# Performance work log

Measured on AMD Instinct MI355X. Metric: run time of the kernel, lower is better.

Reference implementation:

```python
import jax, jax.numpy as jnp
import numpy as np

QMIN = 0.1
EPS = 1e-7
NN, NP_, NE = 200_000, 5_000, 10_000_000


def setup_inputs() -> dict:
    key = jax.random.key(0)
    ks = jax.random.split(key, 8)
    beta = jax.random.uniform(ks[0], (NN,), jnp.float32)
    x = jax.random.normal(ks[1], (NN, 3), jnp.float32)
    isTrack = jax.random.randint(ks[2], (NN,), 0, 2, jnp.int32)
    pt = jax.random.randint(ks[3], (NN,), 0, NP_, jnp.int32)
    noise = jax.random.uniform(ks[4], (NN,)) < 0.1
    parent_target = jnp.where(noise, -1, pt).astype(jnp.int32)
    particle_idx = jnp.arange(NP_, dtype=jnp.int32)
    particle_class = jax.random.randint(ks[5], (NP_,), 0, 5, jnp.int32)
    edge_node = jax.random.randint(ks[6], (NE,), 0, NN, jnp.int32)
    edge_particle = jax.random.randint(ks[7], (NE,), 0, NP_, jnp.int32)
    return {"beta": beta, "x": x, "isTrack": isTrack, "parent_target": parent_target,
            "particle_idx": particle_idx, "particle_class": particle_class,
            "edge_node": edge_node, "edge_particle": edge_particle}


def reference(beta, x, isTrack, parent_target, particle_idx, particle_class, edge_node, edge_particle):
    E = edge_node.shape[0]
    Nn = beta.shape[0]
    Np = particle_idx.shape[0]
    f32 = beta.dtype

    # edge label: node's parent target == particle's idx (ApplyTo*EdgeLabel)
    label = (parent_target[edge_node] == particle_idx[edge_particle]).astype(f32)

    # condensation charge q = arctanh(clamped beta)^2 + qmin
    cb = jnp.clip(beta, EPS, 1.0 - EPS)
    q = jnp.arctanh(cb) ** 2 + QMIN

    # ---- ChildToParent mailbox (masked gathers on edges) ----
    betas = beta[edge_node] * label                              # [E]
    track_m = isTrack[edge_node].astype(f32) * label             # [E]
    pclass_m = particle_class[edge_particle].astype(f32) * label  # [E]
    # where(parent_class < 2, betas, isTrack*betas)
    beta_mail = jnp.where(pclass_m < 2.0, betas, track_m * betas)

    # ---- per-particle max-beta reduction with argmax payload selection ----
    # init 'max beta'/'max q'/'max x' are zeros, concatenated first in the torch code
    max_beta = jax.ops.segment_max(beta_mail, edge_particle, num_segments=Np)
    max_beta = jnp.maximum(max_beta, 0.0)
    hit = (beta_mail == max_beta[edge_particle]) & (max_beta[edge_particle] > 0.0)
    winner = jnp.where(hit, jnp.arange(E, dtype=jnp.int32), -1)
    best_edge = jax.ops.segment_max(winner, edge_particle, num_segments=Np)
    valid = best_edge >= 0
    safe = jnp.maximum(best_edge, 0)
    qs = q[edge_node] * label
    xs = x[edge_node] * label[:, None]
    max_q = jnp.where(valid, qs[safe], 0.0)            # [Np]
    max_x = jnp.where(valid[:, None], xs[safe], 0.0)   # [Np,3]

    # ---- ParentToChild potentials (ParentToChildEF) ----
    diff = max_x[edge_particle] - x[edge_node]          # [E,3]
    dist = jnp.sqrt(jnp.sum(diff * diff, axis=1))       # [E]
    mq = max_q[edge_particle]
    v_attract = 3.0 * label * mq * dist * dist
    v_repulse = (1.0 - label) * jnp.maximum(2.0 - dist, 0.0) * mq

    # ---- sum mailbox to nodes (ParentToChildNF) ----
    attract = jax.ops.segment_sum(v_attract, edge_node, num_segments=Nn)
    repulse = jax.ops.segment_sum(v_repulse, edge_node, num_segments=Nn)
    node_lv = q * (attract + repulse)                   # [Nn]
    return node_lv
```

## Files before the change

### kernel.cpp

```cpp
#include <hip/hip_runtime.h>

#define QMIN_V 0.1f
#define EPS_V  1e-7f


__global__ void init_ws_kernel(unsigned long long* __restrict__ packed,
                               float* __restrict__ accum, int np, int nn) {
    int tid = blockIdx.x * blockDim.x + threadIdx.x;
    int stride = gridDim.x * blockDim.x;
    for (int j = tid; j < np; j += stride) packed[j] = 0ULL;
    for (int j = tid; j < nn; j += stride) accum[j] = 0.0f;
}

__global__ void passA_kernel(const int* __restrict__ edge_node,
                             const int* __restrict__ edge_particle,
                             const float* __restrict__ beta,
                             const int* __restrict__ isTrack,
                             const int* __restrict__ parent_target,
                             const int* __restrict__ particle_idx,
                             const int* __restrict__ particle_class,
                             unsigned long long* __restrict__ packed,
                             int ne4, int ne) {
    int tid = blockIdx.x * blockDim.x + threadIdx.x;
    int stride = gridDim.x * blockDim.x;
    for (int i = tid; i < ne4; i += stride) {
        int4 en = reinterpret_cast<const int4*>(edge_node)[i];
        int4 ep = reinterpret_cast<const int4*>(edge_particle)[i];
#pragma unroll
        for (int k = 0; k < 4; ++k) {
            int n = (&en.x)[k];
            int p = (&ep.x)[k];
            int pt = parent_target[n];
            if (pt == particle_idx[p]) {
                float b = beta[n];
                int pc = particle_class[p];
                float bm = (pc < 2) ? b : b * (float)isTrack[n];
                if (bm > 0.0f) {
                    unsigned long long key =
                        ((unsigned long long)__float_as_uint(bm) << 32) |
                        (unsigned int)(i * 4 + k);
                    atomicMax(&packed[p], key);
                }
            }
        }
    }
    for (int e = ne4 * 4 + tid; e < ne; e += stride) {
        int n = edge_node[e];
        int p = edge_particle[e];
        if (parent_target[n] == particle_idx[p]) {
            float b = beta[n];
            int pc = particle_class[p];
            float bm = (pc < 2) ? b : b * (float)isTrack[n];
            if (bm > 0.0f) {
                unsigned long long key =
                    ((unsigned long long)__float_as_uint(bm) << 32) |
                    (unsigned int)e;
                atomicMax(&packed[p], key);
            }
        }
    }
}

__global__ void passP_kernel(const unsigned long long* __restrict__ packed,
                             const int* __restrict__ edge_node,
                             const float* __restrict__ beta,
                             const float* __restrict__ x,
                             float4* __restrict__ maxdata, int np) {
    int p = blockIdx.x * blockDim.x + threadIdx.x;
    if (p >= np) return;
    unsigned long long key = packed[p];
    unsigned int bm_bits = (unsigned int)(key >> 32);
    float4 md = make_float4(0.0f, 0.0f, 0.0f, 0.0f);
    if (bm_bits != 0u) {
        int e = (int)(key & 0xffffffffULL);
        int n = edge_node[e];
        float b = beta[n];
        float cb = fminf(fmaxf(b, EPS_V), 1.0f - EPS_V);
        float a = atanhf(cb);
        md.x = a * a + QMIN_V;
        md.y = x[3 * n + 0];
        md.z = x[3 * n + 1];
        md.w = x[3 * n + 2];
    }
    maxdata[p] = md;
}

__global__ void passB_kernel(const int* __restrict__ edge_node,
                             const int* __restrict__ edge_particle,
                             const float* __restrict__ x,
                             const int* __restrict__ parent_target,
                             const int* __restrict__ particle_idx,
                             const float4* __restrict__ maxdata,
                             float* __restrict__ accum,
                             int ne4, int ne) {
    int tid = blockIdx.x * blockDim.x + threadIdx.x;
    int stride = gridDim.x * blockDim.x;
    for (int i = tid; i < ne4; i += stride) {
        int4 en = reinterpret_cast<const int4*>(edge_node)[i];
        int4 ep = reinterpret_cast<const int4*>(edge_particle)[i];
#pragma unroll
        for (int k = 0; k < 4; ++k) {
            int n = (&en.x)[k];
            int p = (&ep.x)[k];
            float4 md = maxdata[p];
            float mq = md.x;
            if (mq > 0.0f) {
                float dx = md.y - x[3 * n + 0];
                float dy = md.z - x[3 * n + 1];
                float dz = md.w - x[3 * n + 2];
                float dist = sqrtf(dx * dx + dy * dy + dz * dz);
                bool label = (parent_target[n] == particle_idx[p]);
                float v = label ? (3.0f * mq * dist * dist)
                                : (fmaxf(2.0f - dist, 0.0f) * mq);
                if (v != 0.0f) atomicAdd(&accum[n], v);
            }
        }
    }
    for (int e = ne4 * 4 + tid; e < ne; e += stride) {
        int n = edge_node[e];
        int p = edge_particle[e];
        float4 md = maxdata[p];
        float mq = md.x;
        if (mq > 0.0f) {
            float dx = md.y - x[3 * n + 0];
            float dy = md.z - x[3 * n + 1];
            float dz = md.w - x[3 * n + 2];
            float dist = sqrtf(dx * dx + dy * dy + dz * dz);
            bool label = (parent_target[n] == particle_idx[p]);
            float v = label ? (3.0f * mq * dist * dist)
                            : (fmaxf(2.0f - dist, 0.0f) * mq);
            if (v != 0.0f) atomicAdd(&accum[n], v);
        }
    }
}

__global__ void passN_kernel(const float* __restrict__ beta,
                             const float* __restrict__ accum,
                             float* __restrict__ out, int nn) {
    int i = blockIdx.x * blockDim.x + threadIdx.x;
    if (i >= nn) return;
    float b = beta[i];
    float cb = fminf(fmaxf(b, EPS_V), 1.0f - EPS_V);
    float a = atanhf(cb);
    out[i] = (a * a + QMIN_V) * accum[i];
}

extern "C" void kernel_launch(void* const* d_in, const int* in_sizes, int n_in,
                              void* d_out, int out_size, void* d_ws, size_t ws_size,
                              hipStream_t stream) {
    const float* beta           = (const float*)d_in[0];
    const float* x              = (const float*)d_in[1];
    const int*   isTrack        = (const int*)d_in[2];
    const int*   parent_target  = (const int*)d_in[3];
    const int*   particle_idx   = (const int*)d_in[4];
    const int*   particle_class = (const int*)d_in[5];
    const int*   edge_node      = (const int*)d_in[6];
    const int*   edge_particle  = (const int*)d_in[7];
    float* out = (float*)d_out;

    int nn = in_sizes[0];
    int np = in_sizes[4];
    int ne = in_sizes[6];

    char* ws = (char*)d_ws;
    unsigned long long* packed = (unsigned long long*)ws;
    size_t off1 = ((size_t)np * 8 + 15) & ~(size_t)15;
    float4* maxdata = (float4*)(ws + off1);
    size_t off2 = off1 + (size_t)np * 16;
    float* accum = (float*)(ws + off2);

    int ne4 = ne / 4;

    init_ws_kernel<<<256, 256, 0, stream>>>(packed, accum, np, nn);
    passA_kernel<<<2048, 256, 0, stream>>>(edge_node, edge_particle, beta,
                                           isTrack, parent_target, particle_idx,
                                           particle_class, packed, ne4, ne);
    passP_kernel<<<(np + 255) / 256, 256, 0, stream>>>(packed, edge_node, beta,
                                                       x, maxdata, np);
    passB_kernel<<<2048, 256, 0, stream>>>(edge_node, edge_particle, x,
                                           parent_target, particle_idx,
                                           maxdata, accum, ne4, ne);
    passN_kernel<<<(nn + 255) / 256, 256, 0, stream>>>(beta, accum, out, nn);
}
```

Before: 275.4 us.

## Stage particle tables in LDS and pack node x with parent target

Particle_idx and the per-particle max charge are copied into shared memory in each block, so edge passes read them from LDS instead of global gathers. When the workspace is large enough, node coordinates and parent target are packed into one float4 array, and the parent-to-child pass skips loads for particles with zero charge. The first pass now handles 8 edges per iteration with loads batched ahead of use. The cost is an extra prep kernel, a per-block LDS fill of 5000 entries, and a dependence on workspace size.

Result: faster. 233.5 us (-15.2%).

```diff
diff --git a/kernel.cpp b/kernel.cpp
--- a/kernel.cpp
+++ b/kernel.cpp
@@ -12,44 +12,65 @@
     for (int j = tid; j < nn; j += stride) accum[j] = 0.0f;
 }
 
+__global__ void prep_xpt_kernel(const float* __restrict__ x,
+                                const int* __restrict__ pt,
+                                float4* __restrict__ xpt, int nn) {
+    int i = blockIdx.x * blockDim.x + threadIdx.x;
+    if (i >= nn) return;
+    xpt[i] = make_float4(x[3 * i + 0], x[3 * i + 1], x[3 * i + 2],
+                         __int_as_float(pt[i]));
+}
+
 __global__ void passA_kernel(const int* __restrict__ edge_node,
                              const int* __restrict__ edge_particle,
                              const float* __restrict__ beta,
                              const int* __restrict__ isTrack,
-                             const int* __restrict__ parent_target,
-                             const int* __restrict__ particle_idx,
-                             const int* __restrict__ particle_class,
+                             const int* __restrict__ pt,
+                             const int* __restrict__ pidx,
+                             const int* __restrict__ pclass,
                              unsigned long long* __restrict__ packed,
-                             int ne4, int ne) {
+                             int np, int ne8, int ne) {
+    extern __shared__ int s_pidx[];
+    for (int j = threadIdx.x; j < np; j += blockDim.x) s_pidx[j] = pidx[j];
+    __syncthreads();
+
     int tid = blockIdx.x * blockDim.x + threadIdx.x;
     int stride = gridDim.x * blockDim.x;
-    for (int i = tid; i < ne4; i += stride) {
-        int4 en = reinterpret_cast<const int4*>(edge_node)[i];
-        int4 ep = reinterpret_cast<const int4*>(edge_particle)[i];
-#pragma unroll
-        for (int k = 0; k < 4; ++k) {
-            int n = (&en.x)[k];
-            int p = (&ep.x)[k];
-            int pt = parent_target[n];
-            if (pt == particle_idx[p]) {
-                float b = beta[n];
-                int pc = particle_class[p];
-                float bm = (pc < 2) ? b : b * (float)isTrack[n];
+    const int4* en4 = reinterpret_cast<const int4*>(edge_node);
+    const int4* ep4 = reinterpret_cast<const int4*>(edge_particle);
+
+    for (int i = tid; i < ne8; i += stride) {
+        int4 a0 = en4[2 * i], a1 = en4[2 * i + 1];
+        int4 b0 = ep4[2 * i], b1 = ep4[2 * i + 1];
+        int n[8] = {a0.x, a0.y, a0.z, a0.w, a1.x, a1.y, a1.z, a1.w};
+        int p[8] = {b0.x, b0.y, b0.z, b0.w, b1.x, b1.y, b1.z, b1.w};
+        int t[8];
+#pragma unroll
+        for (int k = 0; k < 8; ++k) t[k] = pt[n[k]];
+        int q[8];
+#pragma unroll
+        for (int k = 0; k < 8; ++k) q[k] = s_pidx[p[k]];
+#pragma unroll
+        for (int k = 0; k < 8; ++k) {
+            if (t[k] == q[k]) {
+                float b = beta[n[k]];
+                int pc = pclass[p[k]];
+                float bm = (pc < 2) ? b : b * (float)isTrack[n[k]];
                 if (bm > 0.0f) {
                     unsigned long long key =
                         ((unsigned long long)__float_as_uint(bm) << 32) |
-                        (unsigned int)(i * 4 + k);
-                    atomicMax(&packed[p], key);
+                        (unsigned int)(8 * i + k);
+                    atomicMax(&packed[p[k]], key);
                 }
             }
         }
     }
-    for (int e = ne4 * 4 + tid; e < ne; e += stride) {
+    for (int e = ne8 * 8 + tid; e < ne; e += stride) {
         int n = edge_node[e];
         int p = edge_particle[e];
-        if (parent_target[n] == particle_idx[p]) {
+        if (pt[n] == pidx[p]) {
             float b = beta[n];
-            int pc = particle_class[p];
+            int pc = pclass[p];
             float bm = (pc < 2) ? b : b * (float)isTrack[n];
             if (bm > 0.0f) {
                 unsigned long long key =
@@ -65,70 +86,109 @@
                              const int* __restrict__ edge_node,
                              const float* __restrict__ beta,
                              const float* __restrict__ x,
-                             float4* __restrict__ maxdata, int np) {
+                             const int* __restrict__ pidx,
+                             float4* __restrict__ maxdata,
+                             float* __restrict__ mq, int np) {
     int p = blockIdx.x * blockDim.x + threadIdx.x;
     if (p >= np) return;
     unsigned long long key = packed[p];
     unsigned int bm_bits = (unsigned int)(key >> 32);
-    float4 md = make_float4(0.0f, 0.0f, 0.0f, 0.0f);
+    float mqv = 0.0f, mx = 0.0f, my = 0.0f, mz = 0.0f;
     if (bm_bits != 0u) {
         int e = (int)(key & 0xffffffffULL);
         int n = edge_node[e];
         float b = beta[n];
         float cb = fminf(fmaxf(b, EPS_V), 1.0f - EPS_V);
         float a = atanhf(cb);
-        md.x = a * a + QMIN_V;
-        md.y = x[3 * n + 0];
-        md.z = x[3 * n + 1];
-        md.w = x[3 * n + 2];
-    }
-    maxdata[p] = md;
-}
-
+        mqv = a * a + QMIN_V;
+        mx = x[3 * n + 0];
+        my = x[3 * n + 1];
+        mz = x[3 * n + 2];
+    }
+    maxdata[p] = make_float4(mx, my, mz, __int_as_float(pidx[p]));
+    mq[p] = mqv;
+}
+
+template <int USE_XPT>
 __global__ void passB_kernel(const int* __restrict__ edge_node,
                              const int* __restrict__ edge_particle,
                              const float* __restrict__ x,
-                             const int* __restrict__ parent_target,
-                             const int* __restrict__ particle_idx,
+                             const int* __restrict__ pt,
+                             const float4* __restrict__ xpt,
                              const float4* __restrict__ maxdata,
+                             const float* __restrict__ mq,
                              float* __restrict__ accum,
-                             int ne4, int ne) {
+                             int np, int ne4, int ne) {
+    extern __shared__ float s_mq[];
+    for (int j = threadIdx.x; j < np; j += blockDim.x) s_mq[j] = mq[j];
+    __syncthreads();
+
     int tid = blockIdx.x * blockDim.x + threadIdx.x;
     int stride = gridDim.x * blockDim.x;
+    const int4* en4 = reinterpret_cast<const int4*>(edge_node);
+    const int4* ep4 = reinterpret_cast<const int4*>(edge_particle);
+
     for (int i = tid; i < ne4; i += stride) {
-        int4 en = reinterpret_cast<const int4*>(edge_node)[i];
-        int4 ep = reinterpret_cast<const int4*>(edge_particle)[i];
+        int4 a = en4[i];
+        int4 b = ep4[i];
+        int n[4] = {a.x, a.y, a.z, a.w};
+        int p[4] = {b.x, b.y, b.z, b.w};
+        float m[4];
+#pragma unroll
+        for (int k = 0; k < 4; ++k) m[k] = s_mq[p[k]];
+        float4 md[4];
+        float xv0[4], xv1[4], xv2[4];
+        int ptv[4];
 #pragma unroll
         for (int k = 0; k < 4; ++k) {
-            int n = (&en.x)[k];
-            int p = (&ep.x)[k];
-            float4 md = maxdata[p];
-            float mq = md.x;
-            if (mq > 0.0f) {
-                float dx = md.y - x[3 * n + 0];
-                float dy = md.z - x[3 * n + 1];
-                float dz = md.w - x[3 * n + 2];
-                float dist = sqrtf(dx * dx + dy * dy + dz * dz);
-                bool label = (parent_target[n] == particle_idx[p]);
-                float v = label ? (3.0f * mq * dist * dist)
-                                : (fmaxf(2.0f - dist, 0.0f) * mq);
-                if (v != 0.0f) atomicAdd(&accum[n], v);
+            if (m[k] > 0.0f) {
+                md[k] = maxdata[p[k]];
+                if (USE_XPT) {
+                    float4 xp = xpt[n[k]];
+                    xv0[k] = xp.x; xv1[k] = xp.y; xv2[k] = xp.z;
+                    ptv[k] = __float_as_int(xp.w);
+                } else {
+                    xv0[k] = x[3 * n[k] + 0];
+                    xv1[k] = x[3 * n[k] + 1];
+                    xv2[k] = x[3 * n[k] + 2];
+                    ptv[k] = pt[n[k]];
+                }
+            }
+        }
+#pragma unroll
+        for (int k = 0; k < 4; ++k) {
+            if (m[k] > 0.0f) {
+                float dx = md[k].x - xv0[k];
+                float dy = md[k].y - xv1[k];
+                float dz = md[k].z - xv2[k];
+                float d2 = dx * dx + dy * dy + dz * dz;
+                bool label = (ptv[k] == __float_as_int(md[k].w));
+                float v;
+                if (label) v = 3.0f * m[k] * d2;
+                else       v = fmaxf(2.0f - sqrtf(d2), 0.0f) * m[k];
+                if (v != 0.0f) atomicAdd(&accum[n[k]], v);
             }
         }
     }
     for (int e = ne4 * 4 + tid; e < ne; e += stride) {
         int n = edge_node[e];
         int p = edge_particle[e];
-        float4 md = maxdata[p];
-        float mq = md.x;
-        if (mq > 0.0f) {
-            float dx = md.y - x[3 * n + 0];
-            float dy = md.z - x[3 * n + 1];
-            float dz = md.w - x[3 * n + 2];
-            float dist = sqrtf(dx * dx + dy * dy + dz * dz);
-            bool label = (parent_target[n] == particle_idx[p]);
-            float v = label ? (3.0f * mq * dist * dist)
-                            : (fmaxf(2.0f - dist, 0.0f) * mq);
+        float m = s_mq[p];
+        if (m > 0.0f) {
+            float4 md = maxdata[p];
+            float x0, x1, x2; int ptv;
+            if (USE_XPT) {
+                float4 xp = xpt[n];
+                x0 = xp.x; x1 = xp.y; x2 = xp.z; ptv = __float_as_int(xp.w);
+            } else {
+                x0 = x[3 * n + 0]; x1 = x[3 * n + 1]; x2 = x[3 * n + 2];
+                ptv = pt[n];
+            }
+            float dx = md.x - x0, dy = md.y - x1, dz = md.z - x2;
+            float d2 = dx * dx + dy * dy + dz * dz;
+            bool label = (ptv == __float_as_int(md.w));
+            float v = label ? (3.0f * m * d2)
+                            : (fmaxf(2.0f - sqrtf(d2), 0.0f) * m);
             if (v != 0.0f) atomicAdd(&accum[n], v);
         }
     }
@@ -148,14 +208,14 @@
 extern "C" void kernel_launch(void* const* d_in, const int* in_sizes, int n_in,
                               void* d_out, int out_size, void* d_ws, size_t ws_size,
                               hipStream_t stream) {
-    const float* beta           = (const float*)d_in[0];
-    const float* x              = (const float*)d_in[1];
-    const int*   isTrack        = (const int*)d_in[2];
-    const int*   parent_target  = (const int*)d_in[3];
-    const int*   particle_idx   = (const int*)d_in[4];
-    const int*   particle_class = (const int*)d_in[5];
-    const int*   edge_node      = (const int*)d_in[6];
-    const int*   edge_particle  = (const int*)d_in[7];
+    const float* beta    = (const float*)d_in[0];
+    const float* x       = (const float*)d_in[1];
+    const int*   isTrack = (const int*)d_in[2];
+    const int*   pt      = (const int*)d_in[3];
+    const int*   pidx    = (const int*)d_in[4];
+    const int*   pclass  = (const int*)d_in[5];
+    const int*   en      = (const int*)d_in[6];
+    const int*   ep      = (const int*)d_in[7];
     float* out = (float*)d_out;
 
     int nn = in_sizes[0];
@@ -163,22 +223,37 @@
     int ne = in_sizes[6];
 
     char* ws = (char*)d_ws;
-    unsigned long long* packed = (unsigned long long*)ws;
-    size_t off1 = ((size_t)np * 8 + 15) & ~(size_t)15;
-    float4* maxdata = (float4*)(ws + off1);
-    size_t off2 = off1 + (size_t)np * 16;
-    float* accum = (float*)(ws + off2);
-
+    size_t off = 0;
+    float4* maxdata = (float4*)(ws + off); off += (size_t)np * 16;
+    size_t xpt_off = off;
+    size_t need_xpt = off + (size_t)nn * 16 + (size_t)np * 8 + (size_t)np * 4
+                      + (size_t)nn * 4;
+    bool use_xpt = (ws_size >= need_xpt);
+    float4* xpt = nullptr;
+    if (use_xpt) { xpt = (float4*)(ws + xpt_off); off += (size_t)nn * 16; }
+    unsigned long long* packed = (unsigned long long*)(ws + off); off += (size_t)np * 8;
+    float* mq = (float*)(ws + off); off += (size_t)np * 4;
+    float* accum = (float*)(ws + off);
+
+    int ne8 = ne / 8;
     int ne4 = ne / 4;
+    int lds_bytes = np * (int)sizeof(int);
 
     init_ws_kernel<<<256, 256, 0, stream>>>(packed, accum, np, nn);
-    passA_kernel<<<2048, 256, 0, stream>>>(edge_node, edge_particle, beta,
-                                           isTrack, parent_target, particle_idx,
-                                           particle_class, packed, ne4, ne);
-    passP_kernel<<<(np + 255) / 256, 256, 0, stream>>>(packed, edge_node, beta,
-                                                       x, maxdata, np);
-    passB_kernel<<<2048, 256, 0, stream>>>(edge_node, edge_particle, x,
-                                           parent_target, particle_idx,
-                                           maxdata, accum, ne4, ne);
+    if (use_xpt)
+        prep_xpt_kernel<<<(nn + 255) / 256, 256, 0, stream>>>(x, pt, xpt, nn);
+    passA_kernel<<<2048, 256, lds_bytes, stream>>>(en, ep, beta, isTrack, pt,
+                                                   pidx, pclass, packed,
+                                                   np, ne8, ne);
+    passP_kernel<<<(np + 255) / 256, 256, 0, stream>>>(packed, en, beta, x,
+                                                       pidx, maxdata, mq, np);
+    if (use_xpt)
+        passB_kernel<1><<<2048, 256, lds_bytes, stream>>>(en, ep, x, pt, xpt,
+                                                          maxdata, mq, accum,
+                                                          np, ne4, ne);
+    else
+        passB_kernel<0><<<2048, 256, lds_bytes, stream>>>(en, ep, x, pt, xpt,
+                                                          maxdata, mq, accum,
+                                                          np, ne4, ne);
     passN_kernel<<<(nn + 255) / 256, 256, 0, stream>>>(beta, accum, out, nn);
 }
```
